# Optimization experiments

Measured on AMD Instinct MI355X. Metric: run time of the kernel, lower is better.

The kernel has to match this reference:

```python
import jax, jax.numpy as jnp
import numpy as np

ALPHA = 0.2  # LeakyReLU negative slope


def _gat_layer(x, W, a):
    """One GraphAttentionLayer (concat=True -> elu output).
    x: (B,N,Din); W: (Din,F); a: (2F,1).
    Faithful to source: adj mask is computed then discarded (softmax over raw e),
    so adj does not enter the math. Uses the additive decomposition
    e_ij = leakyrelu(a1.h_i + a2.h_j) which is mathematically identical to the
    dense (N,N,2F) concat in the original.
    """
    h = x @ W                      # (B,N,F)
    F = W.shape[1]
    a1, a2 = a[:F, 0], a[F:, 0]    # (F,), (F,)
    f1 = h @ a1                    # (B,N)
    f2 = h @ a2                    # (B,N)
    e = jax.nn.leaky_relu(f1[:, :, None] + f2[:, None, :], negative_slope=ALPHA)  # (B,N,N)
    att = jax.nn.softmax(e, axis=-1)
    h_prime = jnp.einsum('bnm,bmf->bnf', att, h)
    return jax.nn.elu(h_prime)


def setup_inputs() -> dict:
    key = jax.random.key(0)
    ks = jax.random.split(key, 6)
    B, N, D, H, F = 8, 1024, 256, 8, 128
    x = jax.random.normal(ks[0], (B, N, D), jnp.float32)
    adj = (jax.random.uniform(ks[1], (N, N)) > 0.9).astype(jnp.float32)
    xavier = lambda fi, fo: 1.414 * (2.0 / (fi + fo)) ** 0.5
    W_heads = jax.random.normal(ks[2], (H, D, F), jnp.float32) * xavier(D, F)
    a_heads = jax.random.normal(ks[3], (H, 2 * F, 1), jnp.float32) * xavier(2 * F, 1)
    W_out = jax.random.normal(ks[4], (H * F, F), jnp.float32) * xavier(H * F, F)
    a_out = jax.random.normal(ks[5], (2 * F, 1), jnp.float32) * xavier(2 * F, 1)
    return {"x": x, "adj": adj, "W_heads": W_heads, "a_heads": a_heads,
            "W_out": W_out, "a_out": a_out}


def reference(x, adj, W_heads, a_heads, W_out, a_out):
    # GAT.forward (dropout omitted: eval mode identity). adj unused per source bug.
    heads = jax.vmap(lambda W, a: _gat_layer(x, W, a))(W_heads, a_heads)  # (H,B,N,F)
    B, N = x.shape[0], x.shape[1]
    xc = jnp.transpose(heads, (1, 2, 0, 3)).reshape(B, N, -1)  # concat heads: (B,N,H*F)
    # out_att has concat=True (applies elu), then GAT.forward applies elu again.
    return jax.nn.elu(_gat_layer(xc, W_out, a_out))
```

## Files before the change

kernel.cpp:

```cpp
#include <hip/hip_runtime.h>
#include <math.h>

#define ALPHA 0.2f
#define LOG2E 1.44269504089f

typedef __attribute__((ext_vector_type(8))) short bf16x8;
typedef __attribute__((ext_vector_type(4))) float f32x4;

__device__ __forceinline__ float elu1(float x)  { return x > 0.f ? x : (__expf(x) - 1.f); }

__device__ __forceinline__ unsigned short f2bf(float x) {
    unsigned u = __float_as_uint(x);
    return (unsigned short)((u + 0x7fffu + ((u >> 16) & 1u)) >> 16);
}
__device__ __forceinline__ unsigned pkbf16(float a, float b) {
    return (unsigned)f2bf(a) | ((unsigned)f2bf(b) << 16);
}
__device__ __forceinline__ float bflo(unsigned v) { return __uint_as_float(v << 16); }
__device__ __forceinline__ float bfhi(unsigned v) { return __uint_as_float(v & 0xffff0000u); }
__device__ __forceinline__ float bfs(unsigned short v) { return __uint_as_float((unsigned)v << 16); }
__device__ __forceinline__ unsigned pkbf_rhu(float a, float b) {
    unsigned ua = __float_as_uint(a) + 0x8000u;
    unsigned ub = __float_as_uint(b) + 0x8000u;
    return __builtin_amdgcn_perm(ub, ua, 0x07060302u);
}

__global__ __launch_bounds__(256) void cvt_w_all(
    const float* __restrict__ Wh, const float* __restrict__ Wo,
    unsigned short* __restrict__ WhT, unsigned short* __restrict__ WoT)
{
    const int z = blockIdx.z;
    const int K = (z < 8) ? 256 : 1024;
    if (blockIdx.x * 64 >= K) return;
    const float* in = (z < 8) ? (Wh + (size_t)z * K * 128) : Wo;
    unsigned short* out = (z < 8) ? (WhT + (size_t)z * 128 * K) : WoT;

    __shared__ float T[64][65];
    const int tid = threadIdx.x;
    const int k0 = blockIdx.x * 64, n0 = blockIdx.y * 64;

    const int kr = tid >> 4, nc = (tid & 15) * 4;
#pragma unroll
    for (int s = 0; s < 4; ++s) {
        float4 v = *(const float4*)(in + (size_t)(k0 + kr + s * 16) * 128 + n0 + nc);
        T[kr + s * 16][nc]     = v.x;
        T[kr + s * 16][nc + 1] = v.y;
        T[kr + s * 16][nc + 2] = v.z;
        T[kr + s * 16][nc + 3] = v.w;
    }
    __syncthreads();
    const int nr0 = tid >> 3, kc = (tid & 7) * 8;
#pragma unroll
    for (int s = 0; s < 2; ++s) {
        int nr = nr0 + s * 32;
        unsigned pk[4];
#pragma unroll
        for (int q = 0; q < 4; ++q)
            pk[q] = pkbf16(T[kc + 2 * q][nr], T[kc + 2 * q + 1][nr]);
        *(uint4*)(out + (size_t)(n0 + nr) * K + k0 + kc) = make_uint4(pk[0], pk[1], pk[2], pk[3]);
    }
}

template <int BM, int BN, int WM, int WN, int DOF, int AF32>
__global__ __launch_bounds__(256) void gemm_t(
    const void* __restrict__ Avp, const unsigned short* __restrict__ Bt,
    unsigned short* __restrict__ Ct, int K,
    const float* __restrict__ aV, float* __restrict__ f1g, float* __restrict__ f2g)
{
    const int RM = WM / 16, RN = WN / 16;
    const int NCA = BM * 8 / 256, NCB = BN * 8 / 256;
    __shared__ __align__(16) unsigned short SAB[(BM + BN) * 72];
    unsigned short (*As)[72] = (unsigned short(*)[72])SAB;
    unsigned short (*Bs)[72] = (unsigned short(*)[72])(SAB + BM * 72);
    unsigned short (*Cs)[BM + 8] = (unsigned short(*)[BM + 8])SAB;
    float* redf = (float*)(SAB + BN * (BM + 8));

    const int tid = threadIdx.x;
    const int w = tid >> 6, lane = tid & 63;
    const int n16 = lane & 15, quad = lane >> 4;
    const int WX = BM / WM;
    const int wm = (w % WX) * WM, wn = (w / WX) * WN;
    const int m0 = blockIdx.x * BM, n0 = blockIdx.y * BN;

    const float* Af = (const float*)Avp;
    const unsigned short* Ab = (const unsigned short*)Avp;
    const int ar = tid >> 2, akc = (tid & 3) * 16;

    f32x4 acc[RM][RN];
#pragma unroll
    for (int mm = 0; mm < RM; ++mm)
#pragma unroll
        for (int nn = 0; nn < RN; ++nn) acc[mm][nn] = (f32x4){0.f, 0.f, 0.f, 0.f};

    uint4 ra[NCA], rb[NCB];
    float4 raf[4];
    if (AF32) {
#pragma unroll
        for (int j = 0; j < 4; ++j)
            raf[j] = *(const float4*)(Af + (size_t)(m0 + ar) * K + akc + 4 * j);
    } else {
#pragma unroll
        for (int i = 0; i < NCA; ++i) {
            int c = tid * NCA + i, r = c >> 3, cc = (c & 7) * 8;
            ra[i] = *(const uint4*)(Ab + (size_t)(m0 + r) * K + cc);
        }
    }
#pragma unroll
    for (int i = 0; i < NCB; ++i) {
        int c = tid * NCB + i, r = c >> 3, cc = (c & 7) * 8;
        rb[i] = *(const uint4*)(Bt + (size_t)(n0 + r) * K + cc);
    }

    const int nk = K >> 6;
    for (int kt = 0; kt < nk; ++kt) {
        __syncthreads();
        if (AF32) {
            uint4 lo = make_uint4(pkbf16(raf[0].x, raf[0].y), pkbf16(raf[0].z, raf[0].w),
                                  pkbf16(raf[1].x, raf[1].y), pkbf16(raf[1].z, raf[1].w));
            uint4 hi = make_uint4(pkbf16(raf[2].x, raf[2].y), pkbf16(raf[2].z, raf[2].w),
                                  pkbf16(raf[3].x, raf[3].y), pkbf16(raf[3].z, raf[3].w));
            *(uint4*)&As[ar][akc]     = lo;
            *(uint4*)&As[ar][akc + 8] = hi;
        } else {
#pragma unroll
            for (int i = 0; i < NCA; ++i) {
                int c = tid * NCA + i, r = c >> 3, cc = (c & 7) * 8;
                *(uint4*)&As[r][cc] = ra[i];
            }
        }
#pragma unroll
        for (int i = 0; i < NCB; ++i) {
            int c = tid * NCB + i, r = c >> 3, cc = (c & 7) * 8;
            *(uint4*)&Bs[r][cc] = rb[i];
        }
        __syncthreads();
        if (kt + 1 < nk) {
            int k0 = (kt + 1) * 64;
            if (AF32) {
#pragma unroll
                for (int j = 0; j < 4; ++j)
                    raf[j] = *(const float4*)(Af + (size_t)(m0 + ar) * K + k0 + akc + 4 * j);
            } else {
#pragma unroll
                for (int i = 0; i < NCA; ++i) {
                    int c = tid * NCA + i, r = c >> 3, cc = (c & 7) * 8;
                    ra[i] = *(const uint4*)(Ab + (size_t)(m0 + r) * K + k0 + cc);
                }
            }
#pragma unroll
            for (int i = 0; i < NCB; ++i) {
                int c = tid * NCB + i, r = c >> 3, cc = (c & 7) * 8;
                rb[i] = *(const uint4*)(Bt + (size_t)(n0 + r) * K + k0 + cc);
            }
        }
#pragma unroll
        for (int ks = 0; ks < 2; ++ks) {
            bf16x8 am[RM], bn[RN];
#pragma unroll
            for (int mm = 0; mm < RM; ++mm)
                am[mm] = *(const bf16x8*)&As[wm + mm * 16 + n16][ks * 32 + quad * 8];
#pragma unroll
            for (int nn = 0; nn < RN; ++nn)
                bn[nn] = *(const bf16x8*)&Bs[wn + nn * 16 + n16][ks * 32 + quad * 8];
#pragma unroll
            for (int mm = 0; mm < RM; ++mm)
#pragma unroll
                for (int nn = 0; nn < RN; ++nn)
                    acc[mm][nn] = __builtin_amdgcn_mfma_f32_16x16x32_bf16(
                        am[mm], bn[nn], acc[mm][nn], 0, 0, 0);
        }
    }

    __syncthreads();

#pragma unroll
    for (int nn = 0; nn < RN; ++nn) {
        int n = wn + nn * 16 + n16;
#pragma unroll
        for (int mm = 0; mm < RM; ++mm) {
            int m = wm + mm * 16 + quad * 4;
            f32x4 a = acc[mm][nn];
            ushort4 o = make_ushort4(f2bf(a[0]), f2bf(a[1]), f2bf(a[2]), f2bf(a[3]));
            *(ushort4*)&Cs[n][m] = o;
        }
    }
    __syncthreads();

    const int CHUNKS = BM * 2 / 16;
    const int RPP = 256 / CHUNKS;
    const int row = tid / CHUNKS, ch = tid % CHUNKS;
#pragma unroll
    for (int s = 0; s < BN / RPP; ++s) {
        int n = row + s * RPP;
        *(uint4*)(Ct + (size_t)(n0 + n) * 8192 + m0 + ch * 8) =
            *(const uint4*)&Cs[n][ch * 8];
    }

    if (DOF) {
        const int mloc = tid & 63, fq = tid >> 6;
        const float* az = aV + blockIdx.y * 256;
        float s1 = 0.f, s2 = 0.f;
#pragma unroll 8
        for (int k = 0; k < 32; ++k) {
            int f = fq * 32 + k;
            float h = bfs(Cs[f][mloc]);
            s1 += h * az[f];
            s2 += h * az[128 + f];
        }
        *(float2*)&redf[(fq * 64 + mloc) * 2] = make_float2(s1, s2);
        __syncthreads();
        if (tid < 64) {
            float a1 = redf[tid * 2]       + redf[(64 + tid) * 2]
                     + redf[(128 + tid) * 2] + redf[(192 + tid) * 2];
            float a2 = redf[tid * 2 + 1]       + redf[(64 + tid) * 2 + 1]
                     + redf[(128 + tid) * 2 + 1] + redf[(192 + tid) * 2 + 1];
            f1g[(size_t)blockIdx.y * 8192 + m0 + tid] = a1;
            f2g[(size_t)blockIdx.y * 8192 + m0 + tid] = a2;
        }
    }
}

__global__ __launch_bounds__(256) void fdot3(
    const unsigned short* __restrict__ hT, const float* __restrict__ a,
    float* __restrict__ f1, float* __restrict__ f2)
{
    __shared__ float4 red[4][64];
    const int tid = threadIdx.x;
    const int fq = tid >> 6, tm = tid & 63;
    const int z = blockIdx.y;
    const int m0 = blockIdx.x * 128 + tm * 2;
    const float* az = a + z * 256;

    float s10 = 0.f, s11 = 0.f, s20 = 0.f, s21 = 0.f;
#pragma unroll 8
    for (int f = fq * 32; f < fq * 32 + 32; ++f) {
        unsigned u = *(const unsigned*)(hT + ((size_t)(z * 128 + f) << 13) + m0);
        float a1 = az[f], a2 = az[128 + f];
        float h0 = bflo(u), h1 = bfhi(u);
        s10 += h0 * a1; s11 += h1 * a1;
        s20 += h0 * a2; s21 += h1 * a2;
    }
    red[fq][tm] = make_float4(s10, s11, s20, s21);
    __syncthreads();
    if (tid < 64) {
        float4 r0 = red[0][tid], r1 = red[1][tid], r2 = red[2][tid], r3 = red[3][tid];
        size_t o = ((size_t)z << 13) + blockIdx.x * 128 + tid * 2;
        *(float2*)(f1 + o) = make_float2(r0.x + r1.x + r2.x + r3.x,
                                         r0.y + r1.y + r2.y + r3.y);
        *(float2*)(f2 + o) = make_float2(r0.z + r1.z + r2.z + r3.z,
                                         r0.w + r1.w + r2.w + r3.w);
    }
}

template <int NI, int OUTBF>
__global__ __launch_bounds__(256) void attn4(
    const unsigned short* __restrict__ hT, const float* __restrict__ f1g,
    const float* __restrict__ f2g, float* __restrict__ outf,
    unsigned short* __restrict__ outb, int elu2)
{
    const int N = 1024, JT = 64, JP = 72;
    __shared__ __align__(16) unsigned short hls[2][128][JP];
    __shared__ float ul[1024], vl[1024];
    __shared__ float wred[4];

    const int tid = threadIdx.x;
    const int w = tid >> 6, lane = tid & 63;
    const int n16 = lane & 15, quad = lane >> 4;
    const int hy = OUTBF ? blockIdx.x : 0;
    const int bz = OUTBF ? blockIdx.z : blockIdx.x;
    const int ibx = blockIdx.y;
    const int hb = hy * 8 + bz;
    const int ITILE = 64 * NI;
    const int iw0 = ibx * ITILE + w * (16 * NI);

    const int j4 = tid * 4;
    {
        float4 fv = *(const float4*)(f2g + (size_t)hb * N + j4);
        fv.x *= LOG2E; fv.y *= LOG2E; fv.z *= LOG2E; fv.w *= LOG2E;
        *(float4*)&ul[j4] = fv;
        float m4 = fmaxf(fmaxf(fv.x, fv.y), fmaxf(fv.z, fv.w));
#pragma unroll
        for (int off = 32; off; off >>= 1) m4 = fmaxf(m4, __shfl_xor(m4, off));
        if (lane == 0) wred[w] = m4;
    }

    float f1L[NI];
#pragma unroll
    for (int ii = 0; ii < NI; ++ii)
        f1L[ii] = f1g[(size_t)hb * N + iw0 + ii * 16 + n16] * LOG2E;

    const unsigned short* gsrc = hT + (size_t)hy * 128 * 8192 + bz * 1024;
    const int sf = tid >> 3, sj = (tid & 7) * 8;

    bf16x8 stg[4];
#pragma unroll
    for (int s = 0; s < 4; ++s)
        stg[s] = *(const bf16x8*)(gsrc + (size_t)(sf + 32 * s) * 8192 + sj);

    __syncthreads();
    const float f2mL = fmaxf(fmaxf(wred[0], wred[1]), fmaxf(wred[2], wred[3]));

    {
        float4 raw = *(const float4*)&ul[j4];
        float4 uu, vv;
        float d0 = raw.x - f2mL, d1 = raw.y - f2mL, d2 = raw.z - f2mL, d3 = raw.w - f2mL;
        uu.x = __builtin_amdgcn_exp2f(d0); vv.x = __builtin_amdgcn_exp2f(ALPHA * d0);
        uu.y = __builtin_amdgcn_exp2f(d1); vv.y = __builtin_amdgcn_exp2f(ALPHA * d1);
        uu.z = __builtin_amdgcn_exp2f(d2); vv.z = __builtin_amdgcn_exp2f(ALPHA * d2);
        uu.w = __builtin_amdgcn_exp2f(d3); vv.w = __builtin_amdgcn_exp2f(ALPHA * d3);
        *(float4*)&ul[j4] = uu;
        *(float4*)&vl[j4] = vv;
    }

    float ri[NI];
#pragma unroll
    for (int ii = 0; ii < NI; ++ii)
        ri[ii] = __builtin_amdgcn_exp2f((ALPHA - 1.f) * (f1L[ii] + f2mL));

    f32x4 acc[NI][8], accl[NI];
#pragma unroll
    for (int ii = 0; ii < NI; ++ii) {
        accl[ii] = (f32x4){0.f, 0.f, 0.f, 0.f};
#pragma unroll
        for (int t = 0; t < 8; ++t) acc[ii][t] = (f32x4){0.f, 0.f, 0.f, 0.f};
    }
    bf16x8 ones;
    { union { bf16x8 v; unsigned u[4]; } o;
      o.u[0] = o.u[1] = o.u[2] = o.u[3] = 0x3F803F80u; ones = o.v; }

#pragma unroll
    for (int s = 0; s < 4; ++s)
        *(bf16x8*)&hls[0][sf + 32 * s][sj] = stg[s];
    __syncthreads();

    for (int jt = 0; jt < N / JT; ++jt) {
        const int cur = jt & 1;
        if (jt + 1 < N / JT) {
            int j0n = (jt + 1) * JT;
#pragma unroll
            for (int s = 0; s < 4; ++s)
                stg[s] = *(const bf16x8*)(gsrc + (size_t)(sf + 32 * s) * 8192 + j0n + sj);
        }
        const int j0 = jt * JT;
#pragma unroll
        for (int kk = 0; kk < 2; ++kk) {
            const int jb = j0 + kk * 32 + quad * 8;
            float4 u0 = *(const float4*)&ul[jb], u1 = *(const float4*)&ul[jb + 4];
            float4 v0 = *(const float4*)&vl[jb], v1 = *(const float4*)&vl[jb + 4];
            float uj[8] = {u0.x, u0.y, u0.z, u0.w, u1.x, u1.y, u1.z, u1.w};
            float vj[8] = {v0.x, v0.y, v0.z, v0.w, v1.x, v1.y, v1.z, v1.w};

            bf16x8 afr[NI];
#pragma unroll
            for (int ii = 0; ii < NI; ++ii) {
                union { bf16x8 v; unsigned u[4]; } cvt;
#pragma unroll
                for (int q = 0; q < 4; ++q) {
                    float p0 = fmaxf(uj[2 * q],     ri[ii] * vj[2 * q]);
                    float p1 = fmaxf(uj[2 * q + 1], ri[ii] * vj[2 * q + 1]);
                    cvt.u[q] = pkbf_rhu(p0, p1);
                }
                afr[ii] = cvt.v;
            }
#pragma unroll
            for (int t = 0; t < 8; ++t) {
                bf16x8 bfr = *(const bf16x8*)&hls[cur][t * 16 + n16][kk * 32 + quad * 8];
#pragma unroll
                for (int ii = 0; ii < NI; ++ii)
                    acc[ii][t] = __builtin_amdgcn_mfma_f32_16x16x32_bf16(
                        afr[ii], bfr, acc[ii][t], 0, 0, 0);
            }
#pragma unroll
            for (int ii = 0; ii < NI; ++ii)
                accl[ii] = __builtin_amdgcn_mfma_f32_16x16x32_bf16(
                    afr[ii], ones, accl[ii], 0, 0, 0);
        }
        if (jt + 1 < N / JT) {
#pragma unroll
            for (int s = 0; s < 4; ++s)
                *(bf16x8*)&hls[1 - cur][sf + 32 * s][sj] = stg[s];
        }
        __syncthreads();
    }

#pragma unroll
    for (int ii = 0; ii < NI; ++ii) {
#pragma unroll
        for (int r = 0; r < 4; ++r) {
            float inv = 1.f / accl[ii][r];
            int i = iw0 + ii * 16 + quad * 4 + r;
#pragma unroll
            for (int t = 0; t < 8; ++t) {
                float tv = acc[ii][t][r] * inv;
                tv = elu1(tv);
                if (OUTBF) {
                    outb[(size_t)(bz * 1024 + i) * 1024 + hy * 128 + t * 16 + n16] = f2bf(tv);
                } else {
                    if (elu2) tv = elu1(tv);
                    outf[(size_t)(bz * 1024 + i) * 128 + t * 16 + n16] = tv;
                }
            }
        }
    }
}

extern "C" void kernel_launch(void* const* d_in, const int* in_sizes, int n_in,
                              void* d_out, int out_size, void* d_ws, size_t ws_size,
                              hipStream_t stream)
{
    const float* x  = (const float*)d_in[0];
    const float* Wh = (const float*)d_in[2];
    const float* ah = (const float*)d_in[3];
    const float* Wo = (const float*)d_in[4];
    const float* ao = (const float*)d_in[5];
    float* out = (float*)d_out;

    unsigned short* WhT = (unsigned short*)d_ws;
    unsigned short* WoT = WhT + 262144;
    unsigned short* h1T = WoT + 131072;
    unsigned short* xcb = h1T + 8388608;
    unsigned short* h2T = xcb + 8388608;
    float* f1a  = (float*)(h2T + 1048576);
    float* f2a  = f1a + 65536;
    float* f1b  = f2a + 65536;
    float* f2b  = f1b + 8192;

    cvt_w_all<<<dim3(16, 2, 9), 256, 0, stream>>>(Wh, Wo, WhT, WoT);

    gemm_t<64, 128, 32, 64, 1, 1><<<dim3(128, 8), 256, 0, stream>>>(
        x, WhT, h1T, 256, ah, f1a, f2a);
    attn4<2, 1><<<dim3(8, 8, 8), 256, 0, stream>>>(h1T, f1a, f2a, nullptr, xcb, 0);

    gemm_t<64, 64, 32, 32, 0, 0><<<dim3(128, 2), 256, 0, stream>>>(
        xcb, WoT, h2T, 1024, nullptr, nullptr, nullptr);
    fdot3<<<dim3(64, 1), 256, 0, stream>>>(h2T, ao, f1b, f2b);
    attn4<1, 0><<<dim3(8, 16, 1), 256, 0, stream>>>(h2T, f1b, f2b, out, nullptr, 1);
}
```

Before: 173.4 us.

## Fuse output-layer attention dots into GEMM epilogue and split final attention by feature

The standalone fdot3 kernel is removed. The f1/f2 attention dot products for the output layer are now computed in the epilogue of the second GEMM, which is generalized to any BM. That GEMM is retiled to 32x128 across 256 blocks, so each block holds all 128 features. The final attention kernel gains an NT template parameter and splits the feature dimension across two z-blocks, doubling its grid from 128 blocks to fill more CUs. The cost is that each feature half recomputes the softmax weights and row sums.

Measured after the change: 167.1 us. 1.04x faster.

```diff
diff --git a/kernel.cpp b/kernel.cpp
--- a/kernel.cpp
+++ b/kernel.cpp
@@ -197,69 +197,41 @@
     }
 
     if (DOF) {
-        const int mloc = tid & 63, fq = tid >> 6;
+        const int G = 256 / BM;
+        const int FP = 128 / G;
+        const int mloc = tid % BM, fq = tid / BM;
         const float* az = aV + blockIdx.y * 256;
         float s1 = 0.f, s2 = 0.f;
 #pragma unroll 8
-        for (int k = 0; k < 32; ++k) {
-            int f = fq * 32 + k;
+        for (int k = 0; k < FP; ++k) {
+            int f = fq * FP + k;
             float h = bfs(Cs[f][mloc]);
             s1 += h * az[f];
             s2 += h * az[128 + f];
         }
-        *(float2*)&redf[(fq * 64 + mloc) * 2] = make_float2(s1, s2);
+        *(float2*)&redf[(fq * BM + mloc) * 2] = make_float2(s1, s2);
         __syncthreads();
-        if (tid < 64) {
-            float a1 = redf[tid * 2]       + redf[(64 + tid) * 2]
-                     + redf[(128 + tid) * 2] + redf[(192 + tid) * 2];
-            float a2 = redf[tid * 2 + 1]       + redf[(64 + tid) * 2 + 1]
-                     + redf[(128 + tid) * 2 + 1] + redf[(192 + tid) * 2 + 1];
+        if (tid < BM) {
+            float a1 = 0.f, a2 = 0.f;
+#pragma unroll
+            for (int g = 0; g < G; ++g) {
+                a1 += redf[(g * BM + tid) * 2];
+                a2 += redf[(g * BM + tid) * 2 + 1];
+            }
             f1g[(size_t)blockIdx.y * 8192 + m0 + tid] = a1;
             f2g[(size_t)blockIdx.y * 8192 + m0 + tid] = a2;
         }
     }
 }
 
-__global__ __launch_bounds__(256) void fdot3(
-    const unsigned short* __restrict__ hT, const float* __restrict__ a,
-    float* __restrict__ f1, float* __restrict__ f2)
-{
-    __shared__ float4 red[4][64];
-    const int tid = threadIdx.x;
-    const int fq = tid >> 6, tm = tid & 63;
-    const int z = blockIdx.y;
-    const int m0 = blockIdx.x * 128 + tm * 2;
-    const float* az = a + z * 256;
-
-    float s10 = 0.f, s11 = 0.f, s20 = 0.f, s21 = 0.f;
-#pragma unroll 8
-    for (int f = fq * 32; f < fq * 32 + 32; ++f) {
-        unsigned u = *(const unsigned*)(hT + ((size_t)(z * 128 + f) << 13) + m0);
-        float a1 = az[f], a2 = az[128 + f];
-        float h0 = bflo(u), h1 = bfhi(u);
-        s10 += h0 * a1; s11 += h1 * a1;
-        s20 += h0 * a2; s21 += h1 * a2;
-    }
-    red[fq][tm] = make_float4(s10, s11, s20, s21);
-    __syncthreads();
-    if (tid < 64) {
-        float4 r0 = red[0][tid], r1 = red[1][tid], r2 = red[2][tid], r3 = red[3][tid];
-        size_t o = ((size_t)z << 13) + blockIdx.x * 128 + tid * 2;
-        *(float2*)(f1 + o) = make_float2(r0.x + r1.x + r2.x + r3.x,
-                                         r0.y + r1.y + r2.y + r3.y);
-        *(float2*)(f2 + o) = make_float2(r0.z + r1.z + r2.z + r3.z,
-                                         r0.w + r1.w + r2.w + r3.w);
-    }
-}
-
-template <int NI, int OUTBF>
+template <int NI, int OUTBF, int NT>
 __global__ __launch_bounds__(256) void attn4(
     const unsigned short* __restrict__ hT, const float* __restrict__ f1g,
     const float* __restrict__ f2g, float* __restrict__ outf,
     unsigned short* __restrict__ outb, int elu2)
 {
     const int N = 1024, JT = 64, JP = 72;
-    __shared__ __align__(16) unsigned short hls[2][128][JP];
+    __shared__ __align__(16) unsigned short hls[2][NT * 16][JP];
     __shared__ float ul[1024], vl[1024];
     __shared__ float wred[4];
 
@@ -268,6 +240,7 @@
     const int n16 = lane & 15, quad = lane >> 4;
     const int hy = OUTBF ? blockIdx.x : 0;
     const int bz = OUTBF ? blockIdx.z : blockIdx.x;
+    const int fz = OUTBF ? 0 : blockIdx.z;
     const int ibx = blockIdx.y;
     const int hb = hy * 8 + bz;
     const int ITILE = 64 * NI;
@@ -289,12 +262,12 @@
     for (int ii = 0; ii < NI; ++ii)
         f1L[ii] = f1g[(size_t)hb * N + iw0 + ii * 16 + n16] * LOG2E;
 
-    const unsigned short* gsrc = hT + (size_t)hy * 128 * 8192 + bz * 1024;
+    const unsigned short* gsrc = hT + (size_t)(hy * 128 + fz * (NT * 16)) * 8192 + bz * 1024;
     const int sf = tid >> 3, sj = (tid & 7) * 8;
 
-    bf16x8 stg[4];
-#pragma unroll
-    for (int s = 0; s < 4; ++s)
+    bf16x8 stg[NT / 2];
+#pragma unroll
+    for (int s = 0; s < NT / 2; ++s)
         stg[s] = *(const bf16x8*)(gsrc + (size_t)(sf + 32 * s) * 8192 + sj);
 
     __syncthreads();
@@ -317,19 +290,19 @@
     for (int ii = 0; ii < NI; ++ii)
         ri[ii] = __builtin_amdgcn_exp2f((ALPHA - 1.f) * (f1L[ii] + f2mL));
 
-    f32x4 acc[NI][8], accl[NI];
+    f32x4 acc[NI][NT], accl[NI];
 #pragma unroll
     for (int ii = 0; ii < NI; ++ii) {
         accl[ii] = (f32x4){0.f, 0.f, 0.f, 0.f};
 #pragma unroll
-        for (int t = 0; t < 8; ++t) acc[ii][t] = (f32x4){0.f, 0.f, 0.f, 0.f};
+        for (int t = 0; t < NT; ++t) acc[ii][t] = (f32x4){0.f, 0.f, 0.f, 0.f};
     }
     bf16x8 ones;
     { union { bf16x8 v; unsigned u[4]; } o;
       o.u[0] = o.u[1] = o.u[2] = o.u[3] = 0x3F803F80u; ones = o.v; }
 
 #pragma unroll
-    for (int s = 0; s < 4; ++s)
+    for (int s = 0; s < NT / 2; ++s)
         *(bf16x8*)&hls[0][sf + 32 * s][sj] = stg[s];
     __syncthreads();
 
@@ -338,7 +311,7 @@
         if (jt + 1 < N / JT) {
             int j0n = (jt + 1) * JT;
 #pragma unroll
-            for (int s = 0; s < 4; ++s)
+            for (int s = 0; s < NT / 2; ++s)
                 stg[s] = *(const bf16x8*)(gsrc + (size_t)(sf + 32 * s) * 8192 + j0n + sj);
         }
         const int j0 = jt * JT;
@@ -363,7 +336,7 @@
                 afr[ii] = cvt.v;
             }
 #pragma unroll
-            for (int t = 0; t < 8; ++t) {
+            for (int t = 0; t < NT; ++t) {
                 bf16x8 bfr = *(const bf16x8*)&hls[cur][t * 16 + n16][kk * 32 + quad * 8];
 #pragma unroll
                 for (int ii = 0; ii < NI; ++ii)
@@ -377,7 +350,7 @@
         }
         if (jt + 1 < N / JT) {
 #pragma unroll
-            for (int s = 0; s < 4; ++s)
+            for (int s = 0; s < NT / 2; ++s)
                 *(bf16x8*)&hls[1 - cur][sf + 32 * s][sj] = stg[s];
         }
         __syncthreads();
@@ -390,14 +363,14 @@
             float inv = 1.f / accl[ii][r];
             int i = iw0 + ii * 16 + quad * 4 + r;
 #pragma unroll
-            for (int t = 0; t < 8; ++t) {
+            for (int t = 0; t < NT; ++t) {
                 float tv = acc[ii][t][r] * inv;
                 tv = elu1(tv);
                 if (OUTBF) {
                     outb[(size_t)(bz * 1024 + i) * 1024 + hy * 128 + t * 16 + n16] = f2bf(tv);
                 } else {
                     if (elu2) tv = elu1(tv);
-                    outf[(size_t)(bz * 1024 + i) * 128 + t * 16 + n16] = tv;
+                    outf[(size_t)(bz * 1024 + i) * 128 + fz * (NT * 16) + t * 16 + n16] = tv;
                 }
             }
         }
@@ -429,10 +402,9 @@
 
     gemm_t<64, 128, 32, 64, 1, 1><<<dim3(128, 8), 256, 0, stream>>>(
         x, WhT, h1T, 256, ah, f1a, f2a);
-    attn4<2, 1><<<dim3(8, 8, 8), 256, 0, stream>>>(h1T, f1a, f2a, nullptr, xcb, 0);
-
-    gemm_t<64, 64, 32, 32, 0, 0><<<dim3(128, 2), 256, 0, stream>>>(
-        xcb, WoT, h2T, 1024, nullptr, nullptr, nullptr);
-    fdot3<<<dim3(64, 1), 256, 0, stream>>>(h2T, ao, f1b, f2b);
-    attn4<1, 0><<<dim3(8, 16, 1), 256, 0, stream>>>(h2T, f1b, f2b, out, nullptr, 1);
-}
+    attn4<2, 1, 8><<<dim3(8, 8, 8), 256, 0, stream>>>(h1T, f1a, f2a, nullptr, xcb, 0);
+
+    gemm_t<32, 128, 16, 64, 1, 0><<<dim3(256, 1), 256, 0, stream>>>(
+        xcb, WoT, h2T, 1024, ao, f1b, f2b);
+    attn4<1, 0, 4><<<dim3(8, 16, 2), 256, 0, stream>>>(h2T, f1b, f2b, out, nullptr, 1);
+}
```
